# Optimization experiments

Hardware: AMD Instinct MI355X
Metric: run time of the kernel (lower is better)

## Reference

```python
import jax, jax.numpy as jnp
import numpy as np

N_NODES = 50000
N_EDGES = 500000
D = 128
K_CLUSTERS = 1024  # fixed cluster count for Kongming_Cluster
EPS = 1e-8


def setup_inputs() -> dict:
    key = jax.random.key(0)
    k1, k2, k3, k4 = jax.random.split(key, 4)
    x = jax.random.normal(k1, (N_NODES, D), dtype=jnp.float32)
    edge_index = jax.random.randint(k2, (2, N_EDGES), 0, N_NODES, dtype=jnp.int32)
    W1 = jax.random.normal(k3, (D, D), dtype=jnp.float32) * (1.0 / np.sqrt(D))
    b1 = jax.random.normal(k4, (D,), dtype=jnp.float32) * 0.01
    return {"x": x, "edge_index": edge_index, "W1": W1, "b1": b1}


def reference(x, edge_index, W1, b1):
    src, dst = edge_index[0], edge_index[1]
    # --- SLPropagate: mean aggregation of neighbor features over edge list ---
    msg = x[src]                                               # [E, D] gather
    agg = jax.ops.segment_sum(msg, dst, num_segments=N_NODES)  # [N, D] scatter-add
    deg = jax.ops.segment_sum(jnp.ones((N_EDGES,), x.dtype), dst, num_segments=N_NODES)
    h = agg / jnp.maximum(deg, 1.0)[:, None]                   # [N, D]

    # --- Kongming_Cluster: cosine-similarity assignment to K centroids ---
    hn = h / (jnp.linalg.norm(h, axis=-1, keepdims=True) + EPS)  # row-normalized
    centroids = hn[:K_CLUSTERS]                                  # [K, D]
    sim = hn @ centroids.T                                       # [N, K] cosine sims
    assign = jnp.argmax(sim, axis=-1)                            # [N] cluster index
    counts = jax.ops.segment_sum(jnp.ones((N_NODES,), x.dtype), assign,
                                 num_segments=K_CLUSTERS)
    xc = jax.ops.segment_sum(h, assign, num_segments=K_CLUSTERS)
    xc = xc / jnp.maximum(counts, 1.0)[:, None]                  # [K, D] cluster means

    # --- lin1 on compressed representation ---
    y = xc @ W1.T + b1                                           # [K, D]

    # --- Kongming_Reconstruct: scatter/gather back to per-node rows ---
    out = y[assign]                                              # [N, D]
    return out
```

## Files before the change

### kernel.cpp

```cpp
#include <hip/hip_runtime.h>

#define N_NODES 50000
#define N_EDGES 500000
#define DIM 128
#define KC 1024
#define CAP 64
#define EPSV 1e-8f
#define LO_SCALE 4096.0f
#define INV_LO_SCALE (1.0f / 4096.0f)
#define NSPLIT 2

typedef _Float16 f16x8 __attribute__((ext_vector_type(8)));
typedef _Float16 f16x4 __attribute__((ext_vector_type(4)));
typedef _Float16 f16x2 __attribute__((ext_vector_type(2)));
typedef float f32x4 __attribute__((ext_vector_type(4)));

__device__ __forceinline__ unsigned ford(float f) {
    unsigned b = __float_as_uint(f);
    return (b & 0x80000000u) ? ~b : (b | 0x80000000u);
}

__global__ void fill_buckets_k(const int* __restrict__ ei, int* __restrict__ bucket,
                               int* __restrict__ cursor) {
    int e = blockIdx.x * blockDim.x + threadIdx.x;
    if (e >= N_EDGES) return;
    int src = ei[e];
    int dst = ei[N_EDGES + e];
    int pos = atomicAdd(cursor + dst, 1);
    if (pos < CAP) bucket[dst * CAP + pos] = src;
}

__global__ void agg_norm_k(const float* __restrict__ x, const int* __restrict__ bucket,
                           const int* __restrict__ cursor, float* __restrict__ h,
                           _Float16* __restrict__ Ahi, _Float16* __restrict__ Alo) {
    const int lane = threadIdx.x & 63;
    const int wv = threadIdx.x >> 6;
    const int half = lane >> 5, q = lane & 31;
    const int n = blockIdx.x * 8 + wv * 2 + half;

    int cnt_mine = cursor[n];
    if (cnt_mine > CAP) cnt_mine = CAP;
    int cnt_other = __shfl_xor(cnt_mine, 32);
    int cmax = max(cnt_mine, cnt_other);

    if (cmax <= 32) {
        int v = (q < cnt_mine) ? bucket[n * CAP + q] : 0x7fffffff;
#pragma unroll
        for (int k = 2; k <= 32; k <<= 1) {
#pragma unroll
            for (int j = k >> 1; j >= 1; j >>= 1) {
                int other = __shfl_xor(v, j);
                bool lower = ((q & j) == 0);
                bool asc = ((q & k) == 0);
                int mn = min(v, other), mx = max(v, other);
                v = (lower == asc) ? mn : mx;
            }
        }
        const float4* x4p = (const float4*)x;
        float4 a4 = make_float4(0.f, 0.f, 0.f, 0.f);
        const int base = half << 5;
        for (int j = 0; j < cmax; j += 2) {
            int s0 = __shfl(v, base + j);
            int s1 = __shfl(v, base + j + 1);
            if (j < cnt_mine) {
                float4 t = x4p[(size_t)s0 * 32 + q];
                a4.x += t.x; a4.y += t.y; a4.z += t.z; a4.w += t.w;
            }
            if (j + 1 < cnt_mine) {
                float4 t = x4p[(size_t)s1 * 32 + q];
                a4.x += t.x; a4.y += t.y; a4.z += t.z; a4.w += t.w;
            }
        }
        float inv = 1.0f / (float)(cnt_mine > 0 ? cnt_mine : 1);
        float4 h4;
        h4.x = a4.x * inv; h4.y = a4.y * inv; h4.z = a4.z * inv; h4.w = a4.w * inv;
        float ss = h4.x * h4.x + h4.y * h4.y + h4.z * h4.z + h4.w * h4.w;
#pragma unroll
        for (int o = 1; o < 32; o <<= 1) ss += __shfl_xor(ss, o);
        float sc = 1.0f / (sqrtf(ss) + EPSV);
        float4 hn4;
        hn4.x = h4.x * sc; hn4.y = h4.y * sc; hn4.z = h4.z * sc; hn4.w = h4.w * sc;

        ((float4*)h)[(size_t)n * 32 + q] = h4;
        _Float16 h0 = (_Float16)hn4.x, h1 = (_Float16)hn4.y;
        _Float16 h2 = (_Float16)hn4.z, h3 = (_Float16)hn4.w;
        f16x4 ph = {h0, h1, h2, h3};
        f16x4 pl = {(_Float16)((hn4.x - (float)h0) * LO_SCALE),
                    (_Float16)((hn4.y - (float)h1) * LO_SCALE),
                    (_Float16)((hn4.z - (float)h2) * LO_SCALE),
                    (_Float16)((hn4.w - (float)h3) * LO_SCALE)};
        *(f16x4*)(Ahi + (size_t)n * DIM + q * 4) = ph;
        *(f16x4*)(Alo + (size_t)n * DIM + q * 4) = pl;
    } else {
        for (int tt = 0; tt < 2; ++tt) {
            int nn = blockIdx.x * 8 + wv * 2 + tt;
            int cnt = cursor[nn];
            if (cnt > CAP) cnt = CAP;
            int v = (lane < cnt) ? bucket[nn * CAP + lane] : 0x7fffffff;
#pragma unroll
            for (int k = 2; k <= 64; k <<= 1) {
#pragma unroll
                for (int j = k >> 1; j >= 1; j >>= 1) {
                    int other = __shfl_xor(v, j);
                    bool lower = ((lane & j) == 0);
                    bool asc = ((lane & k) == 0);
                    int mn = min(v, other), mx = max(v, other);
                    v = (lower == asc) ? mn : mx;
                }
            }
            const float2* x2 = (const float2*)x;
            float ax = 0.f, ay = 0.f;
            for (int j = 0; j < cnt; ++j) {
                int s = __shfl(v, j);
                float2 t = x2[(size_t)s * 64 + lane];
                ax += t.x; ay += t.y;
            }
            float degf = (float)(cnt > 0 ? cnt : 1);
            float hx = ax / degf, hy = ay / degf;
            float ss = hx * hx + hy * hy;
#pragma unroll
            for (int o = 1; o < 64; o <<= 1) ss += __shfl_xor(ss, o);
            float denom = sqrtf(ss) + EPSV;
            float hnx = hx / denom, hny = hy / denom;
            ((float2*)h)[(size_t)nn * 64 + lane] = make_float2(hx, hy);
            _Float16 hix = (_Float16)hnx, hiy = (_Float16)hny;
            f16x2 ph; ph[0] = hix; ph[1] = hiy;
            f16x2 pl; pl[0] = (_Float16)((hnx - (float)hix) * LO_SCALE);
            pl[1] = (_Float16)((hny - (float)hiy) * LO_SCALE);
            *(f16x2*)(Ahi + (size_t)nn * DIM + lane * 2) = ph;
            *(f16x2*)(Alo + (size_t)nn * DIM + lane * 2) = pl;
        }
    }
}

#define SWZ14(u) ((u) ^ ((((u) >> 8) & 7) << 4))

__global__ __launch_bounds__(256, 3) void sim_mfma7_k(const _Float16* __restrict__ Ahi,
                                                      const _Float16* __restrict__ Alo,
                                                      unsigned long long* __restrict__ part) {
    __shared__ __align__(16) char Bs[2][16384];
    const int lane = threadIdx.x & 63;
    const int wv = threadIdx.x >> 6;
    const int r16 = lane & 15, kg = lane >> 4;
    const int m0 = blockIdx.x * 128 + wv * 32;
    const int cbase = blockIdx.y * 65536;
    const int col0 = blockIdx.y * 512;

    int ar0 = m0 + r16;      if (ar0 > N_NODES - 1) ar0 = N_NODES - 1;
    int ar1 = m0 + 16 + r16; if (ar1 > N_NODES - 1) ar1 = N_NODES - 1;
    f16x8 ah0[4], al0[4], ah1[4], al1[4];
#pragma unroll
    for (int ks = 0; ks < 4; ++ks) {
        size_t o0 = (size_t)ar0 * DIM + ks * 32 + kg * 8;
        size_t o1 = (size_t)ar1 * DIM + ks * 32 + kg * 8;
        ah0[ks] = *(const f16x8*)(Ahi + o0);
        al0[ks] = *(const f16x8*)(Alo + o0);
        ah1[ks] = *(const f16x8*)(Ahi + o1);
        al1[ks] = *(const f16x8*)(Alo + o1);
    }

    const int u0 = wv * 2048 + lane * 16;
    const int u1 = u0 + 1024;
    const int d0 = SWZ14(u0), d1 = SWZ14(u1);
    const int e0 = u0 >> 1, e1 = u1 >> 1;

    float best0_0 = -1e30f, best0_1 = -1e30f, best0_2 = -1e30f, best0_3 = -1e30f;
    float best1_0 = -1e30f, best1_1 = -1e30f, best1_2 = -1e30f, best1_3 = -1e30f;
    int bi0_0 = 0, bi0_1 = 0, bi0_2 = 0, bi0_3 = 0;
    int bi1_0 = 0, bi1_1 = 0, bi1_2 = 0, bi1_3 = 0;

    const int rbase = r16 * 256;
    const int x4 = (r16 & 7) << 4;

    f16x8 sA = *(const f16x8*)(Ahi + cbase + e0);
    f16x8 sB = *(const f16x8*)(Ahi + cbase + e1);
    f16x8 sC = *(const f16x8*)(Alo + cbase + e0);
    f16x8 sD = *(const f16x8*)(Alo + cbase + e1);
    {
        char* bc = &Bs[0][0];
        *(f16x8*)(bc + d0) = sA; *(f16x8*)(bc + d1) = sB;
        *(f16x8*)(bc + 8192 + d0) = sC; *(f16x8*)(bc + 8192 + d1) = sD;
    }
    __syncthreads();

    for (int kc = 0; kc < 16; ++kc) {
        const int cur = kc & 1;
        if (kc < 15) {
            int go = cbase + (kc + 1) * 4096;
            sA = *(const f16x8*)(Ahi + go + e0);
            sB = *(const f16x8*)(Ahi + go + e1);
            sC = *(const f16x8*)(Alo + go + e0);
            sD = *(const f16x8*)(Alo + go + e1);
        }
        char* bc = &Bs[cur][0];
#pragma unroll
        for (int ns = 0; ns < 2; ++ns) {
            f32x4 c1a = (f32x4){0.f, 0.f, 0.f, 0.f};
            f32x4 c2a = (f32x4){0.f, 0.f, 0.f, 0.f};
            f32x4 c1b = (f32x4){0.f, 0.f, 0.f, 0.f};
            f32x4 c2b = (f32x4){0.f, 0.f, 0.f, 0.f};
#pragma unroll
            for (int ks = 0; ks < 4; ++ks) {
                int off = ns * 4096 + rbase + ((ks * 64 + kg * 16) ^ x4);
                f16x8 bh = *(const f16x8*)(bc + off);
                f16x8 bl = *(const f16x8*)(bc + 8192 + off);
                c1a = __builtin_amdgcn_mfma_f32_16x16x32_f16(ah0[ks], bh, c1a, 0, 0, 0);
                c2a = __builtin_amdgcn_mfma_f32_16x16x32_f16(ah0[ks], bl, c2a, 0, 0, 0);
                c2a = __builtin_amdgcn_mfma_f32_16x16x32_f16(al0[ks], bh, c2a, 0, 0, 0);
                c1b = __builtin_amdgcn_mfma_f32_16x16x32_f16(ah1[ks], bh, c1b, 0, 0, 0);
                c2b = __builtin_amdgcn_mfma_f32_16x16x32_f16(ah1[ks], bl, c2b, 0, 0, 0);
                c2b = __builtin_amdgcn_mfma_f32_16x16x32_f16(al1[ks], bh, c2b, 0, 0, 0);
            }
            int col = col0 + kc * 32 + ns * 16 + r16;
            float s;
            s = c1a[0] + c2a[0] * INV_LO_SCALE; if (s > best0_0) { best0_0 = s; bi0_0 = col; }
            s = c1a[1] + c2a[1] * INV_LO_SCALE; if (s > best0_1) { best0_1 = s; bi0_1 = col; }
            s = c1a[2] + c2a[2] * INV_LO_SCALE; if (s > best0_2) { best0_2 = s; bi0_2 = col; }
            s = c1a[3] + c2a[3] * INV_LO_SCALE; if (s > best0_3) { best0_3 = s; bi0_3 = col; }
            s = c1b[0] + c2b[0] * INV_LO_SCALE; if (s > best1_0) { best1_0 = s; bi1_0 = col; }
            s = c1b[1] + c2b[1] * INV_LO_SCALE; if (s > best1_1) { best1_1 = s; bi1_1 = col; }
            s = c1b[2] + c2b[2] * INV_LO_SCALE; if (s > best1_2) { best1_2 = s; bi1_2 = col; }
            s = c1b[3] + c2b[3] * INV_LO_SCALE; if (s > best1_3) { best1_3 = s; bi1_3 = col; }
        }
        if (kc < 15) {
            char* bn = &Bs[cur ^ 1][0];
            *(f16x8*)(bn + d0) = sA; *(f16x8*)(bn + d1) = sB;
            *(f16x8*)(bn + 8192 + d0) = sC; *(f16x8*)(bn + 8192 + d1) = sD;
        }
        __syncthreads();
    }

    float bestA[8] = {best0_0, best0_1, best0_2, best0_3,
                      best1_0, best1_1, best1_2, best1_3};
    int bidxA[8] = {bi0_0, bi0_1, bi0_2, bi0_3, bi1_0, bi1_1, bi1_2, bi1_3};
    unsigned long long* prow = part + (size_t)blockIdx.y * N_NODES;
#pragma unroll
    for (int qq = 0; qq < 8; ++qq) {
        float b = bestA[qq];
        int bi = bidxA[qq];
#pragma unroll
        for (int o = 1; o < 16; o <<= 1) {
            float os = __shfl_xor(b, o);
            int oi = __shfl_xor(bi, o);
            if (os > b || (os == b && oi < bi)) { b = os; bi = oi; }
        }
        if (r16 == 0) {
            int gr = m0 + (qq >> 2) * 16 + kg * 4 + (qq & 3);
            if (gr < N_NODES) {
                prow[gr] = ((unsigned long long)ford(b) << 32) | (unsigned)(KC - 1 - bi);
            }
        }
    }
}

__global__ void decode_count_k(const unsigned long long* __restrict__ part,
                               int* __restrict__ assign, int* __restrict__ counts) {
    int n = blockIdx.x * 256 + threadIdx.x;
    if (n >= N_NODES) return;
    unsigned long long k0 = part[n];
    unsigned long long k1 = part[(size_t)N_NODES + n];
    unsigned long long m = k0 > k1 ? k0 : k1;
    int a = (KC - 1) - (int)(unsigned)(m & 0xFFFFFFFFull);
    assign[n] = a;
    atomicAdd(counts + a, 1);
}

__global__ void scan_k(const int* __restrict__ counts, int* __restrict__ offs,
                       int* __restrict__ ccur) {
    __shared__ int wsum[4];
    int t = threadIdx.x;
    int lane = t & 63, wv = t >> 6;
    int4 v = ((const int4*)counts)[t];
    int s = v.x + v.y + v.z + v.w;
    int ps = s;
#pragma unroll
    for (int o = 1; o < 64; o <<= 1) {
        int u = __shfl_up(ps, o);
        if (lane >= o) ps += u;
    }
    if (lane == 63) wsum[wv] = ps;
    __syncthreads();
    int base = 0;
#pragma unroll
    for (int w = 0; w < 4; ++w) base += (w < wv) ? wsum[w] : 0;
    int excl = base + ps - s;
    int4 o4;
    o4.x = excl;
    o4.y = excl + v.x;
    o4.z = excl + v.x + v.y;
    o4.w = excl + v.x + v.y + v.z;
    ((int4*)offs)[t] = o4;
    ((int4*)ccur)[t] = o4;
}

__global__ void fill_clist_k(const int* __restrict__ assign, int* __restrict__ ccur,
                             int* __restrict__ clist) {
    int n = blockIdx.x * 256 + threadIdx.x;
    if (n >= N_NODES) return;
    int p = atomicAdd(ccur + assign[n], 1);
    clist[p] = n;
}

__global__ void xcy_out_k(const float* __restrict__ h, const int* __restrict__ clist,
                          const int* __restrict__ offs, const int* __restrict__ counts,
                          const float* __restrict__ W1, const float* __restrict__ b1,
                          float* __restrict__ out) {
    __shared__ float xr[DIM];
    int c = blockIdx.x, t = threadIdx.x;
    int s = offs[c], cnt = counts[c];
    float acc = 0.f;
    for (int i = 0; i < cnt; ++i) {
        int n = clist[s + i];
        acc += h[(size_t)n * DIM + t];
    }
    xr[t] = acc / (float)(cnt > 0 ? cnt : 1);
    __syncthreads();

    const float4* w4 = (const float4*)(W1 + t * DIM);
    float a0 = 0.f, a1 = 0.f, a2 = 0.f, a3 = 0.f;
#pragma unroll
    for (int kk = 0; kk < 32; ++kk) {
        float4 w = w4[kk];
        a0 = fmaf(xr[4 * kk + 0], w.x, a0);
        a1 = fmaf(xr[4 * kk + 1], w.y, a1);
        a2 = fmaf(xr[4 * kk + 2], w.z, a2);
        a3 = fmaf(xr[4 * kk + 3], w.w, a3);
    }
    float yv = (a0 + a1) + (a2 + a3) + b1[t];

    for (int i = 0; i < cnt; ++i) {
        int n = clist[s + i];
        out[(size_t)n * DIM + t] = yv;
    }
}

extern "C" void kernel_launch(void* const* d_in, const int* in_sizes, int n_in,
                              void* d_out, int out_size, void* d_ws, size_t ws_size,
                              hipStream_t stream) {
    const float* x  = (const float*)d_in[0];
    const int*   ei = (const int*)d_in[1];
    const float* W1 = (const float*)d_in[2];
    const float* b1 = (const float*)d_in[3];
    float* out = (float*)d_out;

    char* ws = (char*)d_ws;
    float* h      = (float*)(ws);
    int*   bucket = (int*)(ws + 25600000);
    int*   clist  = (int*)(ws + 25600000);
    int*   offs   = (int*)(ws + 25800000);
    int*   ccur   = (int*)(ws + 25804096);
    unsigned long long* part = (unsigned long long*)(ws + 25808192);
    int*   cursor = (int*)(ws + 38400000);
    int*   counts = (int*)(ws + 38600000);
    int*   assign = (int*)(ws + 39128384);

    _Float16* Ahi = (_Float16*)d_out;
    _Float16* Alo = (_Float16*)((char*)d_out + 12800000);

    hipMemsetAsync(ws + 38400000, 0, 204096, stream);

    fill_buckets_k<<<(N_EDGES + 255) / 256, 256, 0, stream>>>(ei, bucket, cursor);
    agg_norm_k<<<N_NODES / 8, 256, 0, stream>>>(x, bucket, cursor, h, Ahi, Alo);
    sim_mfma7_k<<<dim3((N_NODES + 127) / 128, NSPLIT), 256, 0, stream>>>(Ahi, Alo, part);
    decode_count_k<<<(N_NODES + 255) / 256, 256, 0, stream>>>(part, assign, counts);
    scan_k<<<1, 256, 0, stream>>>(counts, offs, ccur);
    fill_clist_k<<<(N_NODES + 255) / 256, 256, 0, stream>>>(assign, ccur, clist);
    xcy_out_k<<<KC, 128, 0, stream>>>(h, clist, offs, counts, W1, b1, out);
}
```

Measured before the change: 185.9 us.

## Drop column split in similarity kernel and fuse argmax decode into it

The similarity kernel no longer splits the 1024 centroids across two grid-y blocks. Each block now loops over all 32 column chunks and writes the final assignment and count atomics directly, so the packed partial-result buffer and the separate decode kernel are removed. This saves one launch and a round trip through global memory. In exchange the grid has half as many blocks (391 versus 782), which lowers parallelism and occupancy on a GPU with many CUs, and each block's serial loop is twice as long.

```diff
diff --git a/kernel.cpp b/kernel.cpp
--- a/kernel.cpp
+++ b/kernel.cpp
@@ -8,17 +8,11 @@
 #define EPSV 1e-8f
 #define LO_SCALE 4096.0f
 #define INV_LO_SCALE (1.0f / 4096.0f)
-#define NSPLIT 2
 
 typedef _Float16 f16x8 __attribute__((ext_vector_type(8)));
 typedef _Float16 f16x4 __attribute__((ext_vector_type(4)));
 typedef _Float16 f16x2 __attribute__((ext_vector_type(2)));
 typedef float f32x4 __attribute__((ext_vector_type(4)));
-
-__device__ __forceinline__ unsigned ford(float f) {
-    unsigned b = __float_as_uint(f);
-    return (b & 0x80000000u) ? ~b : (b | 0x80000000u);
-}
 
 __global__ void fill_buckets_k(const int* __restrict__ ei, int* __restrict__ bucket,
                                int* __restrict__ cursor) {
@@ -135,16 +129,15 @@
 
 #define SWZ14(u) ((u) ^ ((((u) >> 8) & 7) << 4))
 
-__global__ __launch_bounds__(256, 3) void sim_mfma7_k(const _Float16* __restrict__ Ahi,
+__global__ __launch_bounds__(256, 3) void sim_mfma3_k(const _Float16* __restrict__ Ahi,
                                                       const _Float16* __restrict__ Alo,
-                                                      unsigned long long* __restrict__ part) {
+                                                      int* __restrict__ assign,
+                                                      int* __restrict__ counts) {
     __shared__ __align__(16) char Bs[2][16384];
     const int lane = threadIdx.x & 63;
     const int wv = threadIdx.x >> 6;
     const int r16 = lane & 15, kg = lane >> 4;
     const int m0 = blockIdx.x * 128 + wv * 32;
-    const int cbase = blockIdx.y * 65536;
-    const int col0 = blockIdx.y * 512;
 
     int ar0 = m0 + r16;      if (ar0 > N_NODES - 1) ar0 = N_NODES - 1;
     int ar1 = m0 + 16 + r16; if (ar1 > N_NODES - 1) ar1 = N_NODES - 1;
@@ -172,10 +165,10 @@
     const int rbase = r16 * 256;
     const int x4 = (r16 & 7) << 4;
 
-    f16x8 sA = *(const f16x8*)(Ahi + cbase + e0);
-    f16x8 sB = *(const f16x8*)(Ahi + cbase + e1);
-    f16x8 sC = *(const f16x8*)(Alo + cbase + e0);
-    f16x8 sD = *(const f16x8*)(Alo + cbase + e1);
+    f16x8 sA = *(const f16x8*)(Ahi + e0);
+    f16x8 sB = *(const f16x8*)(Ahi + e1);
+    f16x8 sC = *(const f16x8*)(Alo + e0);
+    f16x8 sD = *(const f16x8*)(Alo + e1);
     {
         char* bc = &Bs[0][0];
         *(f16x8*)(bc + d0) = sA; *(f16x8*)(bc + d1) = sB;
@@ -183,10 +176,10 @@
     }
     __syncthreads();
 
-    for (int kc = 0; kc < 16; ++kc) {
+    for (int kc = 0; kc < 32; ++kc) {
         const int cur = kc & 1;
-        if (kc < 15) {
-            int go = cbase + (kc + 1) * 4096;
+        if (kc < 31) {
+            int go = (kc + 1) * 4096;
             sA = *(const f16x8*)(Ahi + go + e0);
             sB = *(const f16x8*)(Ahi + go + e1);
             sC = *(const f16x8*)(Alo + go + e0);
@@ -211,7 +204,7 @@
                 c2b = __builtin_amdgcn_mfma_f32_16x16x32_f16(ah1[ks], bl, c2b, 0, 0, 0);
                 c2b = __builtin_amdgcn_mfma_f32_16x16x32_f16(al1[ks], bh, c2b, 0, 0, 0);
             }
-            int col = col0 + kc * 32 + ns * 16 + r16;
+            int col = kc * 32 + ns * 16 + r16;
             float s;
             s = c1a[0] + c2a[0] * INV_LO_SCALE; if (s > best0_0) { best0_0 = s; bi0_0 = col; }
             s = c1a[1] + c2a[1] * INV_LO_SCALE; if (s > best0_1) { best0_1 = s; bi0_1 = col; }
@@ -222,7 +215,7 @@
             s = c1b[2] + c2b[2] * INV_LO_SCALE; if (s > best1_2) { best1_2 = s; bi1_2 = col; }
             s = c1b[3] + c2b[3] * INV_LO_SCALE; if (s > best1_3) { best1_3 = s; bi1_3 = col; }
         }
-        if (kc < 15) {
+        if (kc < 31) {
             char* bn = &Bs[cur ^ 1][0];
             *(f16x8*)(bn + d0) = sA; *(f16x8*)(bn + d1) = sB;
             *(f16x8*)(bn + 8192 + d0) = sC; *(f16x8*)(bn + 8192 + d1) = sD;
@@ -233,7 +226,6 @@
     float bestA[8] = {best0_0, best0_1, best0_2, best0_3,
                       best1_0, best1_1, best1_2, best1_3};
     int bidxA[8] = {bi0_0, bi0_1, bi0_2, bi0_3, bi1_0, bi1_1, bi1_2, bi1_3};
-    unsigned long long* prow = part + (size_t)blockIdx.y * N_NODES;
 #pragma unroll
     for (int qq = 0; qq < 8; ++qq) {
         float b = bestA[qq];
@@ -247,22 +239,11 @@
         if (r16 == 0) {
             int gr = m0 + (qq >> 2) * 16 + kg * 4 + (qq & 3);
             if (gr < N_NODES) {
-                prow[gr] = ((unsigned long long)ford(b) << 32) | (unsigned)(KC - 1 - bi);
-            }
-        }
-    }
-}
-
-__global__ void decode_count_k(const unsigned long long* __restrict__ part,
-                               int* __restrict__ assign, int* __restrict__ counts) {
-    int n = blockIdx.x * 256 + threadIdx.x;
-    if (n >= N_NODES) return;
-    unsigned long long k0 = part[n];
-    unsigned long long k1 = part[(size_t)N_NODES + n];
-    unsigned long long m = k0 > k1 ? k0 : k1;
-    int a = (KC - 1) - (int)(unsigned)(m & 0xFFFFFFFFull);
-    assign[n] = a;
-    atomicAdd(counts + a, 1);
+                assign[gr] = bi;
+                atomicAdd(counts + bi, 1);
+            }
+        }
+    }
 }
 
 __global__ void scan_k(const int* __restrict__ counts, int* __restrict__ offs,
@@ -349,7 +330,6 @@
     int*   clist  = (int*)(ws + 25600000);
     int*   offs   = (int*)(ws + 25800000);
     int*   ccur   = (int*)(ws + 25804096);
-    unsigned long long* part = (unsigned long long*)(ws + 25808192);
     int*   cursor = (int*)(ws + 38400000);
     int*   counts = (int*)(ws + 38600000);
     int*   assign = (int*)(ws + 39128384);
@@ -361,8 +341,7 @@
 
     fill_buckets_k<<<(N_EDGES + 255) / 256, 256, 0, stream>>>(ei, bucket, cursor);
     agg_norm_k<<<N_NODES / 8, 256, 0, stream>>>(x, bucket, cursor, h, Ahi, Alo);
-    sim_mfma7_k<<<dim3((N_NODES + 127) / 128, NSPLIT), 256, 0, stream>>>(Ahi, Alo, part);
-    decode_count_k<<<(N_NODES + 255) / 256, 256, 0, stream>>>(part, assign, counts);
+    sim_mfma3_k<<<(N_NODES + 127) / 128, 256, 0, stream>>>(Ahi, Alo, assign, counts);
     scan_k<<<1, 256, 0, stream>>>(counts, offs, ccur);
     fill_clist_k<<<(N_NODES + 255) / 256, 256, 0, stream>>>(assign, ccur, clist);
     xcy_out_k<<<KC, 128, 0, stream>>>(h, clist, offs, counts, W1, b1, out);
```

Result: faster. 174.8 us (-5.9%).
